# Optimization experiments

Hardware: AMD Instinct MI355X
Metric: run time of the kernel (lower is better)

The kernel has to match this reference:

```python
import jax, jax.numpy as jnp
import numpy as np
from jax import lax

B, S, E, H, V = 32, 128, 512, 512, 32000


def setup_inputs() -> dict:
    key = jax.random.key(0)
    ks = jax.random.split(key, 12)
    s = 1.0 / np.sqrt(H)
    u = lambda k, shape: jax.random.uniform(k, shape, jnp.float32, -s, s)
    return {
        "inputs": jax.random.randint(ks[0], (B, S), 0, V, dtype=jnp.int32),
        "encoder_outputs": jax.random.normal(ks[1], (B, S, H), jnp.float32),
        "lengths": jnp.full((B,), S, dtype=jnp.int32),
        "h0": jnp.zeros((B, H), jnp.float32),
        "c0": jnp.zeros((B, H), jnp.float32),
        "emb": jax.random.normal(ks[2], (V, E), jnp.float32) * 0.02,
        "W_ih": u(ks[3], (4 * H, E)),
        "W_hh": u(ks[4], (4 * H, H)),
        "b_ih": u(ks[5], (4 * H,)),
        "b_hh": u(ks[6], (4 * H,)),
        "W_out": u(ks[7], (V, H)),
        "b_out": u(ks[8], (V,)),
    }


def _decode(inputs, h0, c0, emb, W_ih, W_hh, b_ih, b_hh, W_out, b_out):
    # Teacher-forced per-step LSTM decode. PyTorch LSTM gate order: i, f, g, o.
    def step(carry, tok):
        h, c = carry                              # [B, H] each
        x = emb[tok]                              # [B, E] embedding lookup
        gates = x @ W_ih.T + b_ih + h @ W_hh.T + b_hh  # [B, 4H]
        i, f, g, o = jnp.split(gates, 4, axis=-1)
        i = jax.nn.sigmoid(i)
        f = jax.nn.sigmoid(f)
        g = jnp.tanh(g)
        o = jax.nn.sigmoid(o)
        c = f * c + i * g
        h = o * jnp.tanh(c)
        logp = jax.nn.log_softmax(h @ W_out.T + b_out, axis=-1)  # [B, V]
        # NLLLoss (mean over batch) against the same step's input token,
        # exactly as the original forward computes it.
        nll = -jnp.take_along_axis(logp, tok[:, None], axis=-1).mean()
        sym = jnp.argmax(logp, axis=-1)           # topk(1) indices
        return (h, c), (nll, sym)

    (_, _), (losses, syms) = lax.scan(step, (h0, c0), inputs.T)  # scan over S
    return losses.sum(), syms.T                   # scalar, [B, S]


def reference(inputs, encoder_outputs, lengths, h0, c0, emb,
              W_ih, W_hh, b_ih, b_hh, W_out, b_out):
    # encoder_outputs / lengths are unused (attention is None; lengths[0] == S).
    loss, symbols = _decode(inputs, h0, c0, emb, W_ih, W_hh, b_ih, b_hh, W_out, b_out)
    return loss, symbols
```

## Files before the change

kernel.cpp:

```cpp
#include <hip/hip_runtime.h>
#include <math.h>

#define B_ 32
#define S_ 128
#define H_ 512
#define V_ 32000
#define G4_ 2048
#define NVT 2000
#define NGB 500
#define RBLK 64

typedef __attribute__((ext_vector_type(8))) short bf8;
typedef __attribute__((ext_vector_type(4))) float f4;
typedef unsigned short us;

__device__ __forceinline__ us f2bf(float x) {
    union { float f; unsigned u; } v; v.f = x;
    unsigned r = v.u + 0x7FFFu + ((v.u >> 16) & 1u);
    return (us)(r >> 16);
}
__device__ __forceinline__ float bf2f(us b) {
    union { unsigned u; float f; } v; v.u = ((unsigned)b) << 16; return v.f;
}
__device__ __forceinline__ float4 ldf4(const float* p) {
    return *reinterpret_cast<const float4*>(p);
}
__device__ __forceinline__ void gload_lds16(const void* g, void* l) {
    __builtin_amdgcn_global_load_lds((const __attribute__((address_space(1))) unsigned*)g,
                                     (__attribute__((address_space(3))) unsigned*)l, 16, 0, 0);
}

__global__ __launch_bounds__(256) void k_wsplit(const float* __restrict__ W,
                                                us* __restrict__ Wph,
                                                us* __restrict__ Wpl) {
    const size_t id = (size_t)blockIdx.x * 256 + threadIdx.x;
    const int lane = (int)(id & 63);
    const size_t fc = id >> 6;
    const int kc = (int)(fc & 15);
    const size_t vt = fc >> 4;
    const size_t r = vt * 16 + (lane & 15);
    const int k0 = kc * 32 + (lane >> 4) * 8;
    const float* src = W + r * H_ + k0;
    bf8 hv, lv;
#pragma unroll
    for (int e = 0; e < 8; ++e) {
        float x = src[e];
        us hb = f2bf(x);
        hv[e] = (short)hb;
        lv[e] = (short)f2bf(x - bf2f(hb));
    }
    *reinterpret_cast<bf8*>(Wph + id * 8) = hv;
    *reinterpret_cast<bf8*>(Wpl + id * 8) = lv;
}

__global__ __launch_bounds__(256) void k_whh3(const float* __restrict__ W,
                                              us* __restrict__ B1,
                                              us* __restrict__ B2,
                                              us* __restrict__ B3) {
    const size_t id = (size_t)blockIdx.x * 256 + threadIdx.x;
    const int lane = (int)(id & 63);
    const size_t fc = id >> 6;
    const int kc = (int)(fc & 15);
    const size_t gt = fc >> 4;
    const int nt = (int)(gt & 1);
    const int g = (int)(gt >> 1);
    const int c = lane & 15;
    const int q = nt * 2 + (c >> 3), nl = c & 7;
    const int row = q * 512 + g * 8 + nl;
    const int k0 = kc * 32 + (lane >> 4) * 8;
    const float* src = W + (size_t)row * H_ + k0;
    bf8 v1, v2, v3;
#pragma unroll
    for (int e = 0; e < 8; ++e) {
        float x = src[e];
        us a1 = f2bf(x);
        float r1 = x - bf2f(a1);
        us a2 = f2bf(r1);
        float r2 = r1 - bf2f(a2);
        v1[e] = (short)a1; v2[e] = (short)a2; v3[e] = (short)f2bf(r2);
    }
    *reinterpret_cast<bf8*>(B1 + id * 8) = v1;
    *reinterpret_cast<bf8*>(B2 + id * 8) = v2;
    *reinterpret_cast<bf8*>(B3 + id * 8) = v3;
}

__global__ __launch_bounds__(256) void k_xw(const int* __restrict__ inputs,
                                            const float* __restrict__ emb,
                                            const float* __restrict__ W_ih,
                                            const float* __restrict__ b_ih,
                                            const float* __restrict__ b_hh,
                                            float* __restrict__ XW) {
    __shared__ float es[16 * H_];
    const int tid = threadIdx.x;
    const int j = blockIdx.x * 256 + tid;
    const int t = blockIdx.y;
    const float bias = b_ih[j] + b_hh[j];
#pragma unroll
    for (int half = 0; half < 2; ++half) {
        __syncthreads();
        for (int idx = tid; idx < 16 * 128; idx += 256) {
            int b = idx >> 7, k4 = (idx & 127) << 2;
            int tok = inputs[(half * 16 + b) * S_ + t];
            *reinterpret_cast<float4*>(&es[b * H_ + k4]) = ldf4(emb + (size_t)tok * H_ + k4);
        }
        __syncthreads();
        float acc[16];
#pragma unroll
        for (int b = 0; b < 16; ++b) acc[b] = 0.f;
        for (int k = 0; k < H_; k += 4) {
            float4 wv = ldf4(W_ih + (size_t)j * H_ + k);
#pragma unroll
            for (int b = 0; b < 16; ++b) {
                float4 xv = *reinterpret_cast<const float4*>(&es[b * H_ + k]);
                acc[b] += wv.x * xv.x + wv.y * xv.y + wv.z * xv.z + wv.w * xv.w;
            }
        }
#pragma unroll
        for (int b = 0; b < 16; ++b)
            XW[(size_t)(t * B_ + half * 16 + b) * G4_ + j] = acc[b] + bias;
    }
}

__global__ __launch_bounds__(256)
void k_recur(const float* __restrict__ h0, const float* __restrict__ c0,
             const us* __restrict__ B1f, const us* __restrict__ B2f,
             const us* __restrict__ B3f, const float* __restrict__ XW,
             us* __restrict__ A1, us* __restrict__ A2,
             us* __restrict__ A3, int* __restrict__ flags) {
    __shared__ us wl1[16384], wl2[16384], wl3[16384];
    __shared__ float glds[32][33];
    const int g = blockIdx.x, tid = threadIdx.x;

    {
        const size_t base = (size_t)g * 16384;
        for (int i = tid; i < 2048; i += 256) {
            reinterpret_cast<uint4*>(wl1)[i] = reinterpret_cast<const uint4*>(B1f + base)[i];
            reinterpret_cast<uint4*>(wl2)[i] = reinterpret_cast<const uint4*>(B2f + base)[i];
            reinterpret_cast<uint4*>(wl3)[i] = reinterpret_cast<const uint4*>(B3f + base)[i];
        }
    }
    const int b = tid >> 3, nl = tid & 7;
    const int n = g * 8 + nl;
    const int kc_w = g >> 2, kg_w = g & 3, half_w = b >> 4, lane_w = kg_w * 16 + (b & 15);
    float c_reg = c0[b * H_ + n];
    float hn = h0[b * H_ + n];

    auto write_frags = [&](int slot, float h) {
        us a1 = f2bf(h);
        float r1 = h - bf2f(a1);
        us a2 = f2bf(r1);
        us a3 = f2bf(r1 - bf2f(a2));
        unsigned v1 = a1, v2 = a2, v3 = a3;
        unsigned q1 = (unsigned)__shfl_xor((int)v1, 1);
        unsigned q2 = (unsigned)__shfl_xor((int)v2, 1);
        unsigned q3 = (unsigned)__shfl_xor((int)v3, 1);
        if ((nl & 1) == 0) {
            const size_t ix = ((((size_t)slot * 16 + kc_w) * 2 + half_w) * 64 + lane_w) * 8 + nl;
            __hip_atomic_store((unsigned*)(A1 + ix), v1 | (q1 << 16),
                               __ATOMIC_RELAXED, __HIP_MEMORY_SCOPE_AGENT);
            __hip_atomic_store((unsigned*)(A2 + ix), v2 | (q2 << 16),
                               __ATOMIC_RELAXED, __HIP_MEMORY_SCOPE_AGENT);
            __hip_atomic_store((unsigned*)(A3 + ix), v3 | (q3 << 16),
                               __ATOMIC_RELAXED, __HIP_MEMORY_SCOPE_AGENT);
        }
    };
    write_frags(0, hn);
    asm volatile("s_waitcnt vmcnt(0)" ::: "memory");
    __syncthreads();
    if (tid == 0)
        __hip_atomic_store(&flags[g * 32], 1, __ATOMIC_RELAXED, __HIP_MEMORY_SCOPE_AGENT);

    const int wv = tid >> 6, lane = tid & 63;
    const int mt = wv >> 1, nt = wv & 1;
    const int cidx = lane & 15;

    for (int t = 0; t < S_; ++t) {
        if (tid < 64) {
            int spins = 0;
            while (__hip_atomic_load(&flags[tid * 32], __ATOMIC_RELAXED,
                                     __HIP_MEMORY_SCOPE_AGENT) < t + 1) {
                __builtin_amdgcn_s_sleep(1);
                if (++spins > (1 << 18)) break;
            }
        }
        __syncthreads();
        f4 acc = {0.f, 0.f, 0.f, 0.f};
        const us* a1p = A1 + ((((size_t)t * 16) * 2 + mt) * 64 + lane) * 8;
        const us* a2p = A2 + ((((size_t)t * 16) * 2 + mt) * 64 + lane) * 8;
        const us* a3p = A3 + ((((size_t)t * 16) * 2 + mt) * 64 + lane) * 8;
        const us* b1p = wl1 + ((size_t)(nt * 16) * 64 + lane) * 8;
        const us* b2p = wl2 + ((size_t)(nt * 16) * 64 + lane) * 8;
        const us* b3p = wl3 + ((size_t)(nt * 16) * 64 + lane) * 8;
#pragma unroll 4
        for (int kc = 0; kc < 16; ++kc) {
            bf8 A1v = *reinterpret_cast<const bf8*>(a1p + (size_t)kc * 1024);
            bf8 A2v = *reinterpret_cast<const bf8*>(a2p + (size_t)kc * 1024);
            bf8 A3v = *reinterpret_cast<const bf8*>(a3p + (size_t)kc * 1024);
            bf8 B1v = *reinterpret_cast<const bf8*>(b1p + (size_t)kc * 512);
            bf8 B2v = *reinterpret_cast<const bf8*>(b2p + (size_t)kc * 512);
            bf8 B3v = *reinterpret_cast<const bf8*>(b3p + (size_t)kc * 512);
            acc = __builtin_amdgcn_mfma_f32_16x16x32_bf16(A1v, B1v, acc, 0, 0, 0);
            acc = __builtin_amdgcn_mfma_f32_16x16x32_bf16(A1v, B2v, acc, 0, 0, 0);
            acc = __builtin_amdgcn_mfma_f32_16x16x32_bf16(A2v, B1v, acc, 0, 0, 0);
            acc = __builtin_amdgcn_mfma_f32_16x16x32_bf16(A2v, B2v, acc, 0, 0, 0);
            acc = __builtin_amdgcn_mfma_f32_16x16x32_bf16(A1v, B3v, acc, 0, 0, 0);
            acc = __builtin_amdgcn_mfma_f32_16x16x32_bf16(A3v, B1v, acc, 0, 0, 0);
        }
#pragma unroll
        for (int r = 0; r < 4; ++r)
            glds[mt * 16 + (lane >> 4) * 4 + r][nt * 16 + cidx] = acc[r];
        __syncthreads();
        const float* xwp = XW + ((size_t)t * B_ + b) * G4_;
        const float s_i = glds[b][nl]      + xwp[0 * 512 + n];
        const float s_f = glds[b][8 + nl]  + xwp[1 * 512 + n];
        const float s_g = glds[b][16 + nl] + xwp[2 * 512 + n];
        const float s_o = glds[b][24 + nl] + xwp[3 * 512 + n];
        const float ig = 1.f / (1.f + expf(-s_i));
        const float fg = 1.f / (1.f + expf(-s_f));
        const float gg = tanhf(s_g);
        const float og = 1.f / (1.f + expf(-s_o));
        c_reg = fg * c_reg + ig * gg;
        hn = og * tanhf(c_reg);
        write_frags(t + 1, hn);
        asm volatile("s_waitcnt vmcnt(0)" ::: "memory");
        __syncthreads();
        if (tid == 0)
            __hip_atomic_store(&flags[g * 32], t + 2, __ATOMIC_RELAXED,
                               __HIP_MEMORY_SCOPE_AGENT);
    }
}

__global__ __launch_bounds__(256, 1) void k_gemm(const int* __restrict__ inputs,
                                                 const us* __restrict__ Ah,
                                                 const us* __restrict__ Al,
                                                 const us* __restrict__ Wph,
                                                 const us* __restrict__ Wpl,
                                                 const float* __restrict__ b_out,
                                                 float* __restrict__ sp) {
    __shared__ us abuf[2][32768];
    __shared__ float slds[B_][68];
    const int tid = threadIdx.x;
    const int w = tid >> 6, lane = tid & 63;
    const int vt = blockIdx.x * 4 + w;
    const int v0 = blockIdx.x * 64;
    const int c = lane & 15, kg = lane >> 4;
    const int bb = tid >> 3, sub = tid & 7;

    bf8 Bh[16], Bl[16];
#pragma unroll
    for (int kc = 0; kc < 16; ++kc) {
        const size_t wb = (((size_t)vt * 16 + kc) * 64 + lane) * 8;
        Bh[kc] = *reinterpret_cast<const bf8*>(Wph + wb);
        Bl[kc] = *reinterpret_cast<const bf8*>(Wpl + wb);
    }
#pragma unroll
    for (int kc = 0; kc < 16; ++kc)
        asm volatile("" : "+v"(Bh[kc]), "+v"(Bl[kc]));

    float bo[8];
#pragma unroll
    for (int q = 0; q < 8; ++q) bo[q] = b_out[v0 + sub * 8 + q];

    auto stage = [&](int slot, int buf) {
        const us* s1 = Ah + (size_t)slot * 16384;
        const us* s2 = Al + (size_t)slot * 16384;
        for (int ch = w; ch < 64; ch += 4) {
            const us* src = (ch < 32 ? s1 + ch * 512 : s2 + (ch - 32) * 512) + lane * 8;
            gload_lds16(src, &abuf[buf][ch * 512]);
        }
    };

    stage(1, 0);
    asm volatile("s_waitcnt vmcnt(0)" ::: "memory");
    __builtin_amdgcn_s_barrier();

    for (int mt = 0; mt < S_; ++mt) {
        const int buf = mt & 1;
        if (mt + 1 < S_) stage(mt + 2, buf ^ 1);
        f4 acc0 = {0.f, 0.f, 0.f, 0.f}, acc1 = {0.f, 0.f, 0.f, 0.f};
#pragma unroll
        for (int kc = 0; kc < 16; ++kc) {
            const int o0 = ((kc * 2 + 0) * 64 + lane) * 8;
            const int o1 = ((kc * 2 + 1) * 64 + lane) * 8;
            bf8 A0h = *reinterpret_cast<const bf8*>(&abuf[buf][o0]);
            bf8 A1h = *reinterpret_cast<const bf8*>(&abuf[buf][o1]);
            bf8 A0l = *reinterpret_cast<const bf8*>(&abuf[buf][16384 + o0]);
            bf8 A1l = *reinterpret_cast<const bf8*>(&abuf[buf][16384 + o1]);
            acc0 = __builtin_amdgcn_mfma_f32_16x16x32_bf16(A0h, Bh[kc], acc0, 0, 0, 0);
            acc1 = __builtin_amdgcn_mfma_f32_16x16x32_bf16(A1h, Bh[kc], acc1, 0, 0, 0);
            acc0 = __builtin_amdgcn_mfma_f32_16x16x32_bf16(A0l, Bh[kc], acc0, 0, 0, 0);
            acc1 = __builtin_amdgcn_mfma_f32_16x16x32_bf16(A1l, Bh[kc], acc1, 0, 0, 0);
            acc0 = __builtin_amdgcn_mfma_f32_16x16x32_bf16(A0h, Bl[kc], acc0, 0, 0, 0);
            acc1 = __builtin_amdgcn_mfma_f32_16x16x32_bf16(A1h, Bl[kc], acc1, 0, 0, 0);
        }
        __builtin_amdgcn_s_barrier();
#pragma unroll
        for (int r = 0; r < 4; ++r) {
            slds[kg * 4 + r][w * 16 + c] = acc0[r];
            slds[16 + kg * 4 + r][w * 16 + c] = acc1[r];
        }
        asm volatile("s_waitcnt lgkmcnt(0)" ::: "memory");
        __builtin_amdgcn_s_barrier();
        const int tok = inputs[bb * S_ + mt];
        float m = -INFINITY, s = 0.f, mv = -INFINITY, tv = -INFINITY;
        int mi = 0x7fffffff;
#pragma unroll
        for (int q = 0; q < 8; ++q) {
            const int vl = sub * 8 + q, v = v0 + vl;
            float x = slds[bb][vl] + bo[q];
            float nm = fmaxf(m, x);
            s = s * __expf(m - nm) + __expf(x - nm);
            m = nm;
            if (x > mv) { mv = x; mi = v; }
            if (v == tok) tv = x;
        }
#pragma unroll
        for (int off = 1; off < 8; off <<= 1) {
            float cm = __shfl_xor(m, off), cs = __shfl_xor(s, off);
            float cmv = __shfl_xor(mv, off), ctv = __shfl_xor(tv, off);
            int cmi = __shfl_xor(mi, off);
            float nm = fmaxf(m, cm);
            s = s * __expf(m - nm) + cs * __expf(cm - nm);
            m = nm;
            if (cmv > mv || (cmv == mv && cmi < mi)) { mv = cmv; mi = cmi; }
            tv = fmaxf(tv, ctv);
        }
        if (sub == 0) {
            float* o = sp + ((size_t)(mt * 32 + bb) * NGB + blockIdx.x) * 5;
            o[0] = m; o[1] = s; o[2] = mv; o[3] = (float)mi; o[4] = tv;
        }
        asm volatile("s_waitcnt vmcnt(0)" ::: "memory");
        __builtin_amdgcn_s_barrier();
    }
}

__global__ __launch_bounds__(256) void k_merge(const float* __restrict__ sp,
                                               float* __restrict__ out,
                                               float* __restrict__ lossbuf) {
    const int tid = threadIdx.x;
    const int mi16 = tid >> 4, l16 = tid & 15;
    const int m = blockIdx.x * 16 + mi16;
    float mm = -INFINITY, s = 0.f, mv = -INFINITY, tv = -INFINITY;
    int ai = 0x7fffffff;
    for (int i = l16; i < NGB; i += 16) {
        const float* o = sp + ((size_t)m * NGB + i) * 5;
        float cm = o[0], cs = o[1], cmv = o[2], ctv = o[4];
        int cmi = (int)o[3];
        float nm = fmaxf(mm, cm);
        s = s * expf(mm - nm) + cs * expf(cm - nm);
        mm = nm;
        if (cmv > mv || (cmv == mv && cmi < ai)) { mv = cmv; ai = cmi; }
        tv = fmaxf(tv, ctv);
    }
#pragma unroll
    for (int off = 1; off < 16; off <<= 1) {
        float cm = __shfl_xor(mm, off), cs = __shfl_xor(s, off);
        float cmv = __shfl_xor(mv, off), ctv = __shfl_xor(tv, off);
        int cmi = __shfl_xor(ai, off);
        float nm = fmaxf(mm, cm);
        s = s * expf(mm - nm) + cs * expf(cm - nm);
        mm = nm;
        if (cmv > mv || (cmv == mv && cmi < ai)) { mv = cmv; ai = cmi; }
        tv = fmaxf(tv, ctv);
    }
    if (l16 == 0) {
        const float logZ = mm + logf(s);
        const int t = m >> 5, b = m & 31;
        out[1 + b * S_ + t] = (float)ai;
        lossbuf[m] = tv - logZ;
    }
}

__global__ __launch_bounds__(256) void k_sum(const float* __restrict__ lossbuf,
                                             float* __restrict__ out) {
    const int tid = threadIdx.x;
    float a = 0.f;
    for (int i = tid; i < B_ * S_; i += 256) a += lossbuf[i];
    __shared__ float red[256];
    red[tid] = a;
    __syncthreads();
    for (int off = 128; off > 0; off >>= 1) {
        if (tid < off) red[tid] += red[tid + off];
        __syncthreads();
    }
    if (tid == 0) out[0] = -red[0] / (float)B_;
}

extern "C" void kernel_launch(void* const* d_in, const int* in_sizes, int n_in,
                              void* d_out, int out_size, void* d_ws, size_t ws_size,
                              hipStream_t stream) {
    const int*   inputs = (const int*)d_in[0];
    const float* h0     = (const float*)d_in[3];
    const float* c0     = (const float*)d_in[4];
    const float* emb    = (const float*)d_in[5];
    const float* W_ih   = (const float*)d_in[6];
    const float* W_hh   = (const float*)d_in[7];
    const float* b_ih   = (const float*)d_in[8];
    const float* b_hh   = (const float*)d_in[9];
    const float* W_out  = (const float*)d_in[10];
    const float* b_out  = (const float*)d_in[11];
    float* out = (float*)d_out;

    char* p = (char*)d_ws;
    auto alloc = [&](size_t bytes) { char* r = p; p += (bytes + 255) & ~255ull; return r; };
    float* lossbuf  = (float*)alloc((size_t)B_ * S_ * 4);
    int*   flags    = (int*)alloc(64 * 32 * 4);
    float* sp       = (float*)alloc((size_t)B_ * S_ * NGB * 5 * 4);
    us* A1  = (us*)alloc((size_t)(S_ + 1) * 16384 * 2);
    us* A2  = (us*)alloc((size_t)(S_ + 1) * 16384 * 2);
    us* A3  = (us*)alloc((size_t)(S_ + 1) * 16384 * 2);
    us* Wph = (us*)alloc((size_t)NVT * 16 * 64 * 8 * 2);
    us* Wpl = (us*)alloc((size_t)NVT * 16 * 64 * 8 * 2);
    us* B1f = (us*)alloc((size_t)RBLK * 16384 * 2);
    us* B2f = (us*)alloc((size_t)RBLK * 16384 * 2);
    us* B3f = (us*)alloc((size_t)RBLK * 16384 * 2);
    float* XW = (float*)alloc((size_t)S_ * B_ * G4_ * 4);

    (void)hipMemsetAsync(flags, 0, 64 * 32 * 4, stream);
    k_wsplit<<<(NVT * 16 * 64) / 256, 256, 0, stream>>>(W_out, Wph, Wpl);
    k_whh3<<<(RBLK * 2 * 16 * 64) / 256, 256, 0, stream>>>(W_hh, B1f, B2f, B3f);
    k_xw<<<dim3(8, S_), 256, 0, stream>>>(inputs, emb, W_ih, b_ih, b_hh, XW);
    k_recur<<<RBLK, 256, 0, stream>>>(h0, c0, B1f, B2f, B3f, XW, A1, A2, A3, flags);
    k_gemm<<<NGB, 256, 0, stream>>>(inputs, A1, A2, Wph, Wpl, b_out, sp);
    k_merge<<<(B_ * S_) / 16, 256, 0, stream>>>(sp, out, lossbuf);
    k_sum<<<1, 256, 0, stream>>>(lossbuf, out);
}
```

Baseline: 1.893 ms.

## Fuse W_out bf16 split into GEMM prologue and double GEMM block width

Removes the separate k_wsplit kernel and its packed Wph/Wpl buffers; each GEMM wave now loads its fp32 W_out rows directly and splits them into hi/lo bf16 register fragments. The GEMM block grows from 4 to 8 waves (128 vocab columns per block, 250 blocks), so each staged A tile in LDS is shared by twice as many vocab tiles and the shuffle reduction now spans 16 lanes. This saves one launch and a full write-then-read of the split weights, but 250 blocks may leave some of the MI355X's CUs idle. The k_merge partial count changes with NGB as well.

```diff
diff --git a/kernel.cpp b/kernel.cpp
--- a/kernel.cpp
+++ b/kernel.cpp
@@ -6,8 +6,7 @@
 #define H_ 512
 #define V_ 32000
 #define G4_ 2048
-#define NVT 2000
-#define NGB 500
+#define NGB 250
 #define RBLK 64
 
 typedef __attribute__((ext_vector_type(8))) short bf8;
@@ -28,29 +27,6 @@
 __device__ __forceinline__ void gload_lds16(const void* g, void* l) {
     __builtin_amdgcn_global_load_lds((const __attribute__((address_space(1))) unsigned*)g,
                                      (__attribute__((address_space(3))) unsigned*)l, 16, 0, 0);
-}
-
-__global__ __launch_bounds__(256) void k_wsplit(const float* __restrict__ W,
-                                                us* __restrict__ Wph,
-                                                us* __restrict__ Wpl) {
-    const size_t id = (size_t)blockIdx.x * 256 + threadIdx.x;
-    const int lane = (int)(id & 63);
-    const size_t fc = id >> 6;
-    const int kc = (int)(fc & 15);
-    const size_t vt = fc >> 4;
-    const size_t r = vt * 16 + (lane & 15);
-    const int k0 = kc * 32 + (lane >> 4) * 8;
-    const float* src = W + r * H_ + k0;
-    bf8 hv, lv;
-#pragma unroll
-    for (int e = 0; e < 8; ++e) {
-        float x = src[e];
-        us hb = f2bf(x);
-        hv[e] = (short)hb;
-        lv[e] = (short)f2bf(x - bf2f(hb));
-    }
-    *reinterpret_cast<bf8*>(Wph + id * 8) = hv;
-    *reinterpret_cast<bf8*>(Wpl + id * 8) = lv;
 }
 
 __global__ __launch_bounds__(256) void k_whh3(const float* __restrict__ W,
@@ -230,28 +206,39 @@
     }
 }
 
-__global__ __launch_bounds__(256, 1) void k_gemm(const int* __restrict__ inputs,
+__global__ __launch_bounds__(512, 1) void k_gemm(const int* __restrict__ inputs,
                                                  const us* __restrict__ Ah,
                                                  const us* __restrict__ Al,
-                                                 const us* __restrict__ Wph,
-                                                 const us* __restrict__ Wpl,
+                                                 const float* __restrict__ Wout,
                                                  const float* __restrict__ b_out,
                                                  float* __restrict__ sp) {
     __shared__ us abuf[2][32768];
-    __shared__ float slds[B_][68];
+    __shared__ float slds[B_][132];
     const int tid = threadIdx.x;
     const int w = tid >> 6, lane = tid & 63;
-    const int vt = blockIdx.x * 4 + w;
-    const int v0 = blockIdx.x * 64;
+    const int vt = blockIdx.x * 8 + w;
+    const int v0 = blockIdx.x * 128;
     const int c = lane & 15, kg = lane >> 4;
-    const int bb = tid >> 3, sub = tid & 7;
+    const int bb = tid >> 4, sub = tid & 15;
 
     bf8 Bh[16], Bl[16];
-#pragma unroll
-    for (int kc = 0; kc < 16; ++kc) {
-        const size_t wb = (((size_t)vt * 16 + kc) * 64 + lane) * 8;
-        Bh[kc] = *reinterpret_cast<const bf8*>(Wph + wb);
-        Bl[kc] = *reinterpret_cast<const bf8*>(Wpl + wb);
+    {
+        const float* wrow = Wout + (size_t)(vt * 16 + c) * H_ + kg * 8;
+#pragma unroll
+        for (int kc = 0; kc < 16; ++kc) {
+            const float* src = wrow + kc * 32;
+            float4 w0 = ldf4(src), w1 = ldf4(src + 4);
+            bf8 hv, lv;
+            float xs[8] = {w0.x, w0.y, w0.z, w0.w, w1.x, w1.y, w1.z, w1.w};
+#pragma unroll
+            for (int e = 0; e < 8; ++e) {
+                us hb = f2bf(xs[e]);
+                hv[e] = (short)hb;
+                lv[e] = (short)f2bf(xs[e] - bf2f(hb));
+            }
+            Bh[kc] = hv;
+            Bl[kc] = lv;
+        }
     }
 #pragma unroll
     for (int kc = 0; kc < 16; ++kc)
@@ -264,7 +251,7 @@
     auto stage = [&](int slot, int buf) {
         const us* s1 = Ah + (size_t)slot * 16384;
         const us* s2 = Al + (size_t)slot * 16384;
-        for (int ch = w; ch < 64; ch += 4) {
+        for (int ch = w; ch < 64; ch += 8) {
             const us* src = (ch < 32 ? s1 + ch * 512 : s2 + (ch - 32) * 512) + lane * 8;
             gload_lds16(src, &abuf[buf][ch * 512]);
         }
@@ -315,7 +302,7 @@
             if (v == tok) tv = x;
         }
 #pragma unroll
-        for (int off = 1; off < 8; off <<= 1) {
+        for (int off = 1; off < 16; off <<= 1) {
             float cm = __shfl_xor(m, off), cs = __shfl_xor(s, off);
             float cmv = __shfl_xor(mv, off), ctv = __shfl_xor(tv, off);
             int cmi = __shfl_xor(mi, off);
@@ -409,19 +396,16 @@
     us* A1  = (us*)alloc((size_t)(S_ + 1) * 16384 * 2);
     us* A2  = (us*)alloc((size_t)(S_ + 1) * 16384 * 2);
     us* A3  = (us*)alloc((size_t)(S_ + 1) * 16384 * 2);
-    us* Wph = (us*)alloc((size_t)NVT * 16 * 64 * 8 * 2);
-    us* Wpl = (us*)alloc((size_t)NVT * 16 * 64 * 8 * 2);
     us* B1f = (us*)alloc((size_t)RBLK * 16384 * 2);
     us* B2f = (us*)alloc((size_t)RBLK * 16384 * 2);
     us* B3f = (us*)alloc((size_t)RBLK * 16384 * 2);
     float* XW = (float*)alloc((size_t)S_ * B_ * G4_ * 4);
 
     (void)hipMemsetAsync(flags, 0, 64 * 32 * 4, stream);
-    k_wsplit<<<(NVT * 16 * 64) / 256, 256, 0, stream>>>(W_out, Wph, Wpl);
     k_whh3<<<(RBLK * 2 * 16 * 64) / 256, 256, 0, stream>>>(W_hh, B1f, B2f, B3f);
     k_xw<<<dim3(8, S_), 256, 0, stream>>>(inputs, emb, W_ih, b_ih, b_hh, XW);
     k_recur<<<RBLK, 256, 0, stream>>>(h0, c0, B1f, B2f, B3f, XW, A1, A2, A3, flags);
-    k_gemm<<<NGB, 256, 0, stream>>>(inputs, A1, A2, Wph, Wpl, b_out, sp);
+    k_gemm<<<NGB, 512, 0, stream>>>(inputs, A1, A2, W_out, b_out, sp);
     k_merge<<<(B_ * S_) / 16, 256, 0, stream>>>(sp, out, lossbuf);
     k_sum<<<1, 256, 0, stream>>>(lossbuf, out);
 }
```

Measured after the change: 1.551 ms. 18.1% less time.
